# Kernel optimization log

Measured on AMD Instinct MI355X. Metric: run time of the kernel, lower is better.

The kernel has to match this reference:

```python
import jax, jax.numpy as jnp
import numpy as np
from jax import lax

L = 41                                  # filter_length
H = 32                                  # hidden_size
XVALS = jnp.arange((-L) // 2, L // 2, dtype=jnp.float32)  # [-21, ..., 19], length 41 (matches torch.arange(-41//2, 41//2))


def _gauss_bank(mu, sig, C):
    # mu, sig, C: [H] -> filter bank [H, L]
    return C[:, None] * jnp.exp(-0.5 * ((XVALS[None, :] - mu[:, None]) / sig[:, None]) ** 2)


def _depthwise(z, filt):
    # z: [T, H], filt: [H, L] -> VALID cross-correlation per channel, [T-L+1, H]
    out = lax.conv_general_dilated(
        z.T[None],                      # [1, H, T] (NCH)
        filt[:, None, :],               # [H, 1, L] (OIH)
        window_strides=(1,), padding='VALID',
        feature_group_count=z.shape[1])
    return out[0].T


def setup_inputs() -> dict:
    key = jax.random.key(0)
    ks = jax.random.split(key, 8)
    T, D = 262144, 256
    x0 = jax.random.normal(ks[0], (T, 128), jnp.float32)
    x1 = jax.random.normal(ks[1], (T, 128), jnp.float32)
    W1 = jax.random.normal(ks[2], (H, D), jnp.float32) * 0.1   # fc1.weight [hidden, input]
    b1 = jax.random.normal(ks[3], (H,), jnp.float32) * 0.1     # fc1.bias
    V2 = jax.random.normal(ks[4], (D, H), jnp.float32)         # raw fc2 weight (Sphere-parametrized)
    b2 = jax.random.normal(ks[5], (D,), jnp.float32) * 0.1     # fc2.bias
    mus = jax.random.normal(ks[6], (2, H), jnp.float32) * 3.0
    sigmas = 1.0 + 2.0 * jax.random.uniform(ks[7], (2, H), jnp.float32)
    scaling = jnp.ones((2, H), jnp.float32)
    return {"x0": x0, "x1": x1, "W1": W1, "b1": b1, "V2": V2,
            "b2": b2, "mus": mus, "sigmas": sigmas, "scaling": scaling}


def reference(x0, x1, W1, b1, V2, b2, mus, sigmas, scaling):
    # Clamp (straight-through in bwd; forward value is clamp(min=1))
    std = jnp.clip(sigmas, 1.0, None)
    d = x0.shape[1]

    # ---- encode: per-region projection then per-channel Gaussian (flipped-mu) filters
    z0 = x0 @ W1[:, :d].T               # [T, H]
    z1 = x1 @ W1[:, d:].T               # [T, H]
    z = (_depthwise(z0, _gauss_bank(-mus[0], std[0], scaling[0]))
         + _depthwise(z1, _gauss_bank(-mus[1], std[1], scaling[1]))
         + b1)                          # [T-L+1, H]

    # ---- decode: Sphere-normalized readout (unit-norm columns of V2)
    W2 = V2 / jnp.linalg.norm(V2, axis=0, keepdims=True)  # [D, H]
    zd0 = _depthwise(z, _gauss_bank(mus[0], std[0], scaling[0]))  # [T-2L+2, H]
    zd1 = _depthwise(z, _gauss_bank(mus[1], std[1], scaling[1]))
    xh0 = zd0 @ W2[:d].T + b2[:d]       # [T-2L+2, d]
    xh1 = zd1 @ W2[d:].T + b2[d:]
    # model is untrained -> returns (zs dict, x_hats dict); flattened as tuple
    return (zd0, zd1, xh0, xh1)
```

## Files before the change

kernel.cpp:

```cpp
#include <hip/hip_runtime.h>
#include <math.h>

#define FL 41
#define NH 32
#define WS_E0  0
#define WS_E1  1312
#define WS_G0  2624
#define WS_G1  3936
#define WS_W2T 5248

__global__ __launch_bounds__(256) void setup_kernel(
    const float* __restrict__ V2, const float* __restrict__ mus,
    const float* __restrict__ sigmas, const float* __restrict__ scaling,
    float* __restrict__ ws)
{
    const int tid = threadIdx.x;
    __shared__ float nrm[NH];
    {
        const int h = tid >> 3;
        const int s = tid & 7;
        float p = 0.f;
        for (int jj = 0; jj < 32; ++jj) {
            const float v = V2[(s + jj*8)*NH + h];
            p += v*v;
        }
        p += __shfl_xor(p, 1, 8);
        p += __shfl_xor(p, 2, 8);
        p += __shfl_xor(p, 4, 8);
        if (s == 0) nrm[h] = sqrtf(p);
    }
    __syncthreads();
    for (int idx = tid; idx < NH*256; idx += 256) {
        int h = idx >> 8, j = idx & 255;
        ws[WS_W2T + idx] = V2[j*NH + h] / nrm[h];
    }
    for (int idx = tid; idx < 4*NH*FL; idx += 256) {
        int bank = idx / (NH*FL);
        int rem  = idx - bank*(NH*FL);
        int h = rem / FL, l = rem - h*FL;
        int r = bank & 1;
        float mu = mus[r*NH + h];
        float sg = fmaxf(sigmas[r*NH + h], 1.0f);
        float C  = scaling[r*NH + h];
        float m  = (bank < 2) ? -mu : mu;
        float x  = (float)(l - 21);
        float dd = (x - m) / sg;
        ws[idx] = C * expf(-0.5f * dd * dd);
    }
}

__global__ __launch_bounds__(256) void proj_kernel(
    const float* __restrict__ x0, const float* __restrict__ x1,
    const float* __restrict__ W1,
    float* __restrict__ z0, float* __restrict__ z1, int T)
{
    __shared__ float xT[2][32][132];
    __shared__ float wT[2][32][36];
    const int tid  = threadIdx.x;
    const int row0 = blockIdx.x * 128;

    const int reg = tid >> 7;
    const int h0  = ((tid >> 5) & 3) * 8;
    const int m   = tid & 31;

    float acc[4][8];
#pragma unroll
    for (int i = 0; i < 4; ++i)
#pragma unroll
        for (int j = 0; j < 8; ++j) acc[i][j] = 0.f;

    for (int kc = 0; kc < 4; ++kc) {
        const int c0 = kc * 32;
#pragma unroll
        for (int r = 0; r < 2; ++r) {
            const float* __restrict__ xp = r ? x1 : x0;
#pragma unroll
            for (int p = 0; p < 4; ++p) {
                const int row = p*32 + (tid >> 3);
                const int c   = (tid & 7) * 4;
                const float4 v = *reinterpret_cast<const float4*>(
                    &xp[(size_t)(row0 + row)*128 + c0 + c]);
                xT[r][c+0][row] = v.x; xT[r][c+1][row] = v.y;
                xT[r][c+2][row] = v.z; xT[r][c+3][row] = v.w;
            }
        }
        {
            const int h = tid >> 3;
            const int c = (tid & 7) * 4;
            const float4 a = *reinterpret_cast<const float4*>(&W1[h*256 + c0 + c]);
            wT[0][c+0][h] = a.x; wT[0][c+1][h] = a.y;
            wT[0][c+2][h] = a.z; wT[0][c+3][h] = a.w;
            const float4 b = *reinterpret_cast<const float4*>(&W1[h*256 + 128 + c0 + c]);
            wT[1][c+0][h] = b.x; wT[1][c+1][h] = b.y;
            wT[1][c+2][h] = b.z; wT[1][c+3][h] = b.w;
        }
        __syncthreads();
#pragma unroll
        for (int c = 0; c < 32; ++c) {
            const float4 xv = *reinterpret_cast<const float4*>(&xT[reg][c][m*4]);
            const float4 wa = *reinterpret_cast<const float4*>(&wT[reg][c][h0]);
            const float4 wb = *reinterpret_cast<const float4*>(&wT[reg][c][h0+4]);
            const float xs[4] = {xv.x, xv.y, xv.z, xv.w};
            const float wv[8] = {wa.x, wa.y, wa.z, wa.w, wb.x, wb.y, wb.z, wb.w};
#pragma unroll
            for (int i = 0; i < 4; ++i)
#pragma unroll
                for (int j = 0; j < 8; ++j) acc[i][j] += xs[i] * wv[j];
        }
        __syncthreads();
    }
    float* __restrict__ zp = reg ? z1 : z0;
#pragma unroll
    for (int i = 0; i < 4; ++i) {
        const size_t r = (size_t)(row0 + m*4 + i) * NH + h0;
        float4 o0 = make_float4(acc[i][0], acc[i][1], acc[i][2], acc[i][3]);
        float4 o1 = make_float4(acc[i][4], acc[i][5], acc[i][6], acc[i][7]);
        *reinterpret_cast<float4*>(&zp[r])   = o0;
        *reinterpret_cast<float4*>(&zp[r+4]) = o1;
    }
}

#define ED_BT 128
#define ED_RS 216
#define ED_ZR 176
__global__ __launch_bounds__(512) void encdec_kernel(
    const float* __restrict__ z0, const float* __restrict__ z1,
    const float* __restrict__ b1, const float* __restrict__ ws,
    float* __restrict__ zd0, float* __restrict__ zd1,
    int T, int T2)
{
    __shared__ float s0[ED_RS][NH];
    __shared__ float s1[ED_RS][NH];
    __shared__ float zt[ED_ZR][NH];
    const int tid = threadIdx.x;
    const int t0  = blockIdx.x * ED_BT;

    for (int idx = tid; idx < ED_RS*NH/4; idx += 512) {
        const int f = idx*4, row = f >> 5, col = f & 31;
        const int gr = t0 + row;
        float4 a = make_float4(0.f,0.f,0.f,0.f);
        float4 b = make_float4(0.f,0.f,0.f,0.f);
        if (gr < T) {
            a = *reinterpret_cast<const float4*>(&z0[(size_t)gr*NH + col]);
            b = *reinterpret_cast<const float4*>(&z1[(size_t)gr*NH + col]);
        }
        *reinterpret_cast<float4*>(&s0[row][col]) = a;
        *reinterpret_cast<float4*>(&s1[row][col]) = b;
    }
    __syncthreads();

    const int h = tid & 31;
    {
        const int g  = tid >> 5;
        const int tb = g * 11;
        float acc[11];
        const float bb = b1[h];
#pragma unroll
        for (int i = 0; i < 11; ++i) acc[i] = bb;
        float fr[FL];
#pragma unroll
        for (int l = 0; l < FL; ++l) fr[l] = ws[WS_E0 + h*FL + l];
#pragma unroll
        for (int s = 0; s < 51; ++s) {
            const float a0 = s0[tb + s][h];
#pragma unroll
            for (int i = 0; i < 11; ++i) {
                const int l = s - i;
                if (l >= 0 && l < FL) acc[i] += a0 * fr[l];
            }
        }
#pragma unroll
        for (int l = 0; l < FL; ++l) fr[l] = ws[WS_E1 + h*FL + l];
#pragma unroll
        for (int s = 0; s < 51; ++s) {
            const float a1 = s1[tb + s][h];
#pragma unroll
            for (int i = 0; i < 11; ++i) {
                const int l = s - i;
                if (l >= 0 && l < FL) acc[i] += a1 * fr[l];
            }
        }
#pragma unroll
        for (int i = 0; i < 11; ++i) zt[tb + i][h] = acc[i];
    }
    __syncthreads();

    {
        const int rr = (tid >> 5) & 1;
        const int g  = tid >> 6;
        const int tb = g * 16;
        float fr[FL];
        const float* __restrict__ fb = ws + (rr ? WS_G1 : WS_G0);
#pragma unroll
        for (int l = 0; l < FL; ++l) fr[l] = fb[h*FL + l];
        float acc[16];
#pragma unroll
        for (int i = 0; i < 16; ++i) acc[i] = 0.f;
#pragma unroll
        for (int s = 0; s < 56; ++s) {
            const float a = zt[tb + s][h];
#pragma unroll
            for (int i = 0; i < 16; ++i) {
                const int l = s - i;
                if (l >= 0 && l < FL) acc[i] += a * fr[l];
            }
        }
        float* __restrict__ zd = rr ? zd1 : zd0;
#pragma unroll
        for (int i = 0; i < 16; ++i) {
            const int t = t0 + tb + i;
            if (t < T2) zd[(size_t)t*NH + h] = acc[i];
        }
    }
}

__global__ __launch_bounds__(512) void readout_kernel(
    const float* __restrict__ zd0, const float* __restrict__ zd1,
    const float* __restrict__ W2T, const float* __restrict__ b2,
    float* __restrict__ xh0, float* __restrict__ xh1, int T2)
{
    __shared__ float w2[NH][260];
    __shared__ float zT[2][NH][66];
    const int tid = threadIdx.x;
    const int t0  = blockIdx.x * 64;

    for (int idx = tid; idx < 2048; idx += 512) {
        const int h = idx >> 6, j = (idx & 63) * 4;
        *reinterpret_cast<float4*>(&w2[h][j]) =
            *reinterpret_cast<const float4*>(&W2T[h*256 + j]);
    }
    for (int idx = tid; idx < 1024; idx += 512) {
        const int r   = idx >> 9;
        const int rem = idx & 511;
        const int tl  = rem >> 3;
        const int hh  = (rem & 7) * 4;
        const int t   = t0 + tl;
        float4 v = make_float4(0.f, 0.f, 0.f, 0.f);
        if (t < T2) {
            const float* __restrict__ zp = r ? zd1 : zd0;
            v = *reinterpret_cast<const float4*>(&zp[(size_t)t*NH + hh]);
        }
        zT[r][hh+0][tl] = v.x; zT[r][hh+1][tl] = v.y;
        zT[r][hh+2][tl] = v.z; zT[r][hh+3][tl] = v.w;
    }
    __syncthreads();

    const int m  = tid & 31;
    const int jq = tid >> 5;
    const int jb = jq * 4;

    float acc[2][16];
#pragma unroll
    for (int k = 0; k < 4; ++k)
#pragma unroll
        for (int c = 0; c < 4; ++c) {
            const float bv = b2[jb + 64*k + c];
            acc[0][4*k+c] = bv;
            acc[1][4*k+c] = bv;
        }

#pragma unroll 4
    for (int h = 0; h < NH; ++h) {
        const float2 za = *reinterpret_cast<const float2*>(&zT[0][h][m*2]);
        const float2 zb = *reinterpret_cast<const float2*>(&zT[1][h][m*2]);
        const float4 w0 = *reinterpret_cast<const float4*>(&w2[h][jb]);
        const float4 w1 = *reinterpret_cast<const float4*>(&w2[h][jb + 64]);
        const float4 w2v= *reinterpret_cast<const float4*>(&w2[h][jb + 128]);
        const float4 w3 = *reinterpret_cast<const float4*>(&w2[h][jb + 192]);
        acc[0][0]  += za.x*w0.x; acc[0][1]  += za.x*w0.y;
        acc[0][2]  += za.x*w0.z; acc[0][3]  += za.x*w0.w;
        acc[0][4]  += za.x*w1.x; acc[0][5]  += za.x*w1.y;
        acc[0][6]  += za.x*w1.z; acc[0][7]  += za.x*w1.w;
        acc[0][8]  += zb.x*w2v.x; acc[0][9]  += zb.x*w2v.y;
        acc[0][10] += zb.x*w2v.z; acc[0][11] += zb.x*w2v.w;
        acc[0][12] += zb.x*w3.x; acc[0][13] += zb.x*w3.y;
        acc[0][14] += zb.x*w3.z; acc[0][15] += zb.x*w3.w;
        acc[1][0]  += za.y*w0.x; acc[1][1]  += za.y*w0.y;
        acc[1][2]  += za.y*w0.z; acc[1][3]  += za.y*w0.w;
        acc[1][4]  += za.y*w1.x; acc[1][5]  += za.y*w1.y;
        acc[1][6]  += za.y*w1.z; acc[1][7]  += za.y*w1.w;
        acc[1][8]  += zb.y*w2v.x; acc[1][9]  += zb.y*w2v.y;
        acc[1][10] += zb.y*w2v.z; acc[1][11] += zb.y*w2v.w;
        acc[1][12] += zb.y*w3.x; acc[1][13] += zb.y*w3.y;
        acc[1][14] += zb.y*w3.z; acc[1][15] += zb.y*w3.w;
    }

#pragma unroll
    for (int i = 0; i < 2; ++i) {
        const int t = t0 + m*2 + i;
        if (t < T2) {
#pragma unroll
            for (int k = 0; k < 4; ++k) {
                float* __restrict__ xp = (k < 2) ? xh0 : xh1;
                const int jl = jb + 64 * (k & 1);
                float4 o = make_float4(acc[i][4*k+0], acc[i][4*k+1],
                                       acc[i][4*k+2], acc[i][4*k+3]);
                *reinterpret_cast<float4*>(&xp[(size_t)t*128 + jl]) = o;
            }
        }
    }
}

extern "C" void kernel_launch(void* const* d_in, const int* in_sizes, int n_in,
                              void* d_out, int out_size, void* d_ws, size_t ws_size,
                              hipStream_t stream)
{
    const float* x0      = (const float*)d_in[0];
    const float* x1      = (const float*)d_in[1];
    const float* W1      = (const float*)d_in[2];
    const float* b1      = (const float*)d_in[3];
    const float* V2      = (const float*)d_in[4];
    const float* b2      = (const float*)d_in[5];
    const float* mus     = (const float*)d_in[6];
    const float* sigmas  = (const float*)d_in[7];
    const float* scaling = (const float*)d_in[8];
    float* out = (float*)d_out;
    float* ws  = (float*)d_ws;

    const int T  = in_sizes[0] / 128;
    const int T2 = T - 80;

    float* zd0 = out;
    float* zd1 = out + (size_t)T2 * NH;
    float* xh0 = out + (size_t)2 * T2 * NH;
    float* xh1 = xh0 + (size_t)T2 * 128;

    float* z0 = xh0;
    float* z1 = xh0 + (size_t)T * NH;

    setup_kernel<<<1, 256, 0, stream>>>(V2, mus, sigmas, scaling, ws);
    proj_kernel<<<T / 128, 256, 0, stream>>>(x0, x1, W1, z0, z1, T);
    encdec_kernel<<<(T2 + ED_BT - 1) / ED_BT, 512, 0, stream>>>(
        z0, z1, b1, ws, zd0, zd1, T, T2);
    readout_kernel<<<(T2 + 63) / 64, 512, 0, stream>>>(zd0, zd1, ws + WS_W2T, b2,
                                                       xh0, xh1, T2);
}
```

Baseline: 658.6 us.

## Retile readout kernel to 128-row tiles with per-region thread mapping

Restructures the readout GEMM so each thread computes 16 time rows by 4 output columns for a single region. z is stored row-major in shared memory and read via broadcast, and the tile size doubles to 128 rows. The aim is fewer LDS loads per FMA, less redundant W2 staging per output, and simpler coalesced stores to one output tensor per wavefront. It raises per-thread register use for 64 accumulators and doubles shared memory for z.

```diff
diff --git a/kernel.cpp b/kernel.cpp
--- a/kernel.cpp
+++ b/kernel.cpp
@@ -214,89 +214,74 @@
     }
 }
 
+#define RO_BT 128
 __global__ __launch_bounds__(512) void readout_kernel(
     const float* __restrict__ zd0, const float* __restrict__ zd1,
     const float* __restrict__ W2T, const float* __restrict__ b2,
     float* __restrict__ xh0, float* __restrict__ xh1, int T2)
 {
-    __shared__ float w2[NH][260];
-    __shared__ float zT[2][NH][66];
+    __shared__ float w2[2][NH][132];
+    __shared__ float sz[2][RO_BT][NH];
     const int tid = threadIdx.x;
-    const int t0  = blockIdx.x * 64;
+    const int t0  = blockIdx.x * RO_BT;
 
     for (int idx = tid; idx < 2048; idx += 512) {
-        const int h = idx >> 6, j = (idx & 63) * 4;
-        *reinterpret_cast<float4*>(&w2[h][j]) =
-            *reinterpret_cast<const float4*>(&W2T[h*256 + j]);
-    }
-    for (int idx = tid; idx < 1024; idx += 512) {
-        const int r   = idx >> 9;
-        const int rem = idx & 511;
-        const int tl  = rem >> 3;
-        const int hh  = (rem & 7) * 4;
-        const int t   = t0 + tl;
+        const int h  = idx >> 6;
+        const int jj = (idx & 63) * 4;
+        const int r  = jj >> 7;
+        const int j  = jj & 127;
+        *reinterpret_cast<float4*>(&w2[r][h][j]) =
+            *reinterpret_cast<const float4*>(&W2T[h*256 + jj]);
+    }
+    for (int idx = tid; idx < 2048; idx += 512) {
+        const int f   = idx * 4;
+        const int r   = f >> 12;
+        const int rem = f & 4095;
+        const int row = rem >> 5, col = rem & 31;
+        const int t   = t0 + row;
         float4 v = make_float4(0.f, 0.f, 0.f, 0.f);
         if (t < T2) {
             const float* __restrict__ zp = r ? zd1 : zd0;
-            v = *reinterpret_cast<const float4*>(&zp[(size_t)t*NH + hh]);
-        }
-        zT[r][hh+0][tl] = v.x; zT[r][hh+1][tl] = v.y;
-        zT[r][hh+2][tl] = v.z; zT[r][hh+3][tl] = v.w;
+            v = *reinterpret_cast<const float4*>(&zp[(size_t)t*NH + col]);
+        }
+        *reinterpret_cast<float4*>(&sz[r][row][col]) = v;
     }
     __syncthreads();
 
-    const int m  = tid & 31;
-    const int jq = tid >> 5;
-    const int jb = jq * 4;
-
-    float acc[2][16];
-#pragma unroll
-    for (int k = 0; k < 4; ++k)
-#pragma unroll
-        for (int c = 0; c < 4; ++c) {
-            const float bv = b2[jb + 64*k + c];
-            acc[0][4*k+c] = bv;
-            acc[1][4*k+c] = bv;
-        }
+    const int j  = (tid & 31) * 4;
+    const int r  = (tid >> 5) & 1;
+    const int rw = tid >> 6;
+
+    float acc[16][4];
+    {
+        const float4 bv = *reinterpret_cast<const float4*>(&b2[r*128 + j]);
+#pragma unroll
+        for (int i = 0; i < 16; ++i) {
+            acc[i][0] = bv.x; acc[i][1] = bv.y;
+            acc[i][2] = bv.z; acc[i][3] = bv.w;
+        }
+    }
 
 #pragma unroll 4
     for (int h = 0; h < NH; ++h) {
-        const float2 za = *reinterpret_cast<const float2*>(&zT[0][h][m*2]);
-        const float2 zb = *reinterpret_cast<const float2*>(&zT[1][h][m*2]);
-        const float4 w0 = *reinterpret_cast<const float4*>(&w2[h][jb]);
-        const float4 w1 = *reinterpret_cast<const float4*>(&w2[h][jb + 64]);
-        const float4 w2v= *reinterpret_cast<const float4*>(&w2[h][jb + 128]);
-        const float4 w3 = *reinterpret_cast<const float4*>(&w2[h][jb + 192]);
-        acc[0][0]  += za.x*w0.x; acc[0][1]  += za.x*w0.y;
-        acc[0][2]  += za.x*w0.z; acc[0][3]  += za.x*w0.w;
-        acc[0][4]  += za.x*w1.x; acc[0][5]  += za.x*w1.y;
-        acc[0][6]  += za.x*w1.z; acc[0][7]  += za.x*w1.w;
-        acc[0][8]  += zb.x*w2v.x; acc[0][9]  += zb.x*w2v.y;
-        acc[0][10] += zb.x*w2v.z; acc[0][11] += zb.x*w2v.w;
-        acc[0][12] += zb.x*w3.x; acc[0][13] += zb.x*w3.y;
-        acc[0][14] += zb.x*w3.z; acc[0][15] += zb.x*w3.w;
-        acc[1][0]  += za.y*w0.x; acc[1][1]  += za.y*w0.y;
-        acc[1][2]  += za.y*w0.z; acc[1][3]  += za.y*w0.w;
-        acc[1][4]  += za.y*w1.x; acc[1][5]  += za.y*w1.y;
-        acc[1][6]  += za.y*w1.z; acc[1][7]  += za.y*w1.w;
-        acc[1][8]  += zb.y*w2v.x; acc[1][9]  += zb.y*w2v.y;
-        acc[1][10] += zb.y*w2v.z; acc[1][11] += zb.y*w2v.w;
-        acc[1][12] += zb.y*w3.x; acc[1][13] += zb.y*w3.y;
-        acc[1][14] += zb.y*w3.z; acc[1][15] += zb.y*w3.w;
-    }
-
-#pragma unroll
-    for (int i = 0; i < 2; ++i) {
-        const int t = t0 + m*2 + i;
+        const float4 w = *reinterpret_cast<const float4*>(&w2[r][h][j]);
+#pragma unroll
+        for (int i = 0; i < 16; ++i) {
+            const float zv = sz[r][rw*16 + i][h];
+            acc[i][0] += zv * w.x;
+            acc[i][1] += zv * w.y;
+            acc[i][2] += zv * w.z;
+            acc[i][3] += zv * w.w;
+        }
+    }
+
+    float* __restrict__ xp = r ? xh1 : xh0;
+#pragma unroll
+    for (int i = 0; i < 16; ++i) {
+        const int t = t0 + rw*16 + i;
         if (t < T2) {
-#pragma unroll
-            for (int k = 0; k < 4; ++k) {
-                float* __restrict__ xp = (k < 2) ? xh0 : xh1;
-                const int jl = jb + 64 * (k & 1);
-                float4 o = make_float4(acc[i][4*k+0], acc[i][4*k+1],
-                                       acc[i][4*k+2], acc[i][4*k+3]);
-                *reinterpret_cast<float4*>(&xp[(size_t)t*128 + jl]) = o;
-            }
+            float4 o = make_float4(acc[i][0], acc[i][1], acc[i][2], acc[i][3]);
+            *reinterpret_cast<float4*>(&xp[(size_t)t*128 + j]) = o;
         }
     }
 }
@@ -332,6 +317,6 @@
     proj_kernel<<<T / 128, 256, 0, stream>>>(x0, x1, W1, z0, z1, T);
     encdec_kernel<<<(T2 + ED_BT - 1) / ED_BT, 512, 0, stream>>>(
         z0, z1, b1, ws, zd0, zd1, T, T2);
-    readout_kernel<<<(T2 + 63) / 64, 512, 0, stream>>>(zd0, zd1, ws + WS_W2T, b2,
-                                                       xh0, xh1, T2);
-}
+    readout_kernel<<<(T2 + RO_BT - 1) / RO_BT, 512, 0, stream>>>(
+        zd0, zd1, ws + WS_W2T, b2, xh0, xh1, T2);
+}
```

After: 647.5 us. Within noise of the previous version (-1.7%).
